# Performance work log

Hardware: AMD Instinct MI355X
Metric: run time of the kernel (lower is better)

The kernel has to match this reference:

```python
import jax, jax.numpy as jnp
import numpy as np

N, S, D = 4, 2048, 1024
H, HD = 16, 64
DF = 3 * D
EPS = 1e-5

def _layernorm(x, g, b):
    mu = jnp.mean(x, axis=-1, keepdims=True)
    var = jnp.mean((x - mu) ** 2, axis=-1, keepdims=True)
    return (x - mu) * jax.lax.rsqrt(var + EPS) * g + b

def _pos_embed(s, d, dtype):
    pos = jnp.arange(s, dtype=dtype)                      # (S,)
    i = jnp.arange(d, dtype=dtype)                        # (D,)
    ang = pos[:, None] / (10000.0 ** (2.0 * i / d))       # (S,D)
    pe = jnp.where((jnp.arange(d) % 2) == 0, jnp.sin(ang), jnp.cos(ang))
    return pe

def setup_inputs() -> dict:
    key = jax.random.key(0)
    ks = jax.random.split(key, 12)
    def w(k, shape, fan_in):
        return jax.random.normal(k, shape, dtype=jnp.float32) * (fan_in ** -0.5)
    return {
        "x":  jax.random.normal(ks[0], (N, S, D), dtype=jnp.float32),
        "Wq": w(ks[1], (D, H * HD), D),
        "Wk": w(ks[2], (D, H * HD), D),
        "Wv": w(ks[3], (D, H * HD), D),
        "Wo": w(ks[4], (H * HD, D), H * HD),
        "W1": w(ks[5], (D, DF), D),
        "b1": jnp.zeros((DF,), dtype=jnp.float32),
        "W2": w(ks[6], (DF, D), DF),
        "b2": jnp.zeros((D,), dtype=jnp.float32),
        "g1": jnp.ones((D,), dtype=jnp.float32),
        "be1": jnp.zeros((D,), dtype=jnp.float32),
        "g2": jnp.ones((D,), dtype=jnp.float32),
        "be2": jnp.zeros((D,), dtype=jnp.float32),
    }

def reference(x, Wq, Wk, Wv, Wo, W1, b1, W2, b2, g1, be1, g2, be2):
    n, s, d = x.shape
    # positional encoding (added to x; note original scales scores by model_dim**0.5)
    x = x + _pos_embed(s, d, x.dtype)[None, :, :]
    # MHA on norm1(x)
    h = _layernorm(x, g1, be1)
    q = (h @ Wq).reshape(n, s, H, HD)
    k = (h @ Wk).reshape(n, s, H, HD)
    v = (h @ Wv).reshape(n, s, H, HD)
    scores = jnp.einsum('bqhd,bkhd->bhqk', q, k) / jnp.sqrt(jnp.asarray(d, x.dtype))
    attn = jax.nn.softmax(scores, axis=-1)
    o = jnp.einsum('bhqk,bkhd->bqhd', attn, v).reshape(n, s, H * HD)
    x = x + o @ Wo
    # FFN on norm2(x): Linear -> LeakyReLU(0.01) -> Linear (dropout = identity in eval)
    h2 = _layernorm(x, g2, be2)
    f = jax.nn.leaky_relu(h2 @ W1 + b1, negative_slope=0.01)
    x = x + (f @ W2 + b2)
    return x
```

## Files before the change

kernel.cpp:

```cpp
#include <hip/hip_runtime.h>

typedef unsigned short u16;
typedef __bf16 bf16x8 __attribute__((ext_vector_type(8)));
typedef float f32x4 __attribute__((ext_vector_type(4)));

__device__ __forceinline__ u16 f2bf(float f) {
  unsigned u = __builtin_bit_cast(unsigned, f);
  u += 0x7FFFu + ((u >> 16) & 1u);
  return (u16)(u >> 16);
}

#define GLOAD16(g, l) __builtin_amdgcn_global_load_lds( \
    (const __attribute__((address_space(1))) unsigned int*)(const void*)(g), \
    (__attribute__((address_space(3))) unsigned int*)(void*)(l), 16, 0, 0)

#define SW(r, c) (((r) << 6) + ((((c) ^ ((r) & 7))) << 3))

__global__ __launch_bounds__(256) void tconv(const float* __restrict__ W,
                                             u16* __restrict__ Wt, int K, int N) {
  __shared__ float t[32][33];
  int n0 = blockIdx.x * 32, k0 = blockIdx.y * 32;
  int tx = threadIdx.x, ty = threadIdx.y;
#pragma unroll
  for (int j = 0; j < 4; ++j)
    t[ty + j * 8][tx] = W[(size_t)(k0 + ty + j * 8) * N + n0 + tx];
  __syncthreads();
#pragma unroll
  for (int j = 0; j < 4; ++j)
    Wt[(size_t)(n0 + ty + j * 8) * K + k0 + tx] = f2bf(t[tx][ty + j * 8]);
}

template <bool PE>
__global__ __launch_bounds__(256) void ln_row(const float* __restrict__ in,
                                              const float* __restrict__ g,
                                              const float* __restrict__ be,
                                              float* __restrict__ xout,
                                              u16* __restrict__ hout) {
  const int row = blockIdx.x;
  const int tid = threadIdx.x;
  const int s = row & 2047;
  float4 xv = *(const float4*)&in[(size_t)row * 1024 + tid * 4];
  float vals[4];
  const float* xp = (const float*)&xv;
#pragma unroll
  for (int j = 0; j < 4; ++j) {
    float v = xp[j];
    if (PE) {
      int d = tid * 4 + j;
      float freq = powf(10000.f, -2.f * (float)d * (1.f / 1024.f));
      float ang = (float)s * freq;
      v += (d & 1) ? cosf(ang) : sinf(ang);
    }
    vals[j] = v;
  }
  if (PE) {
    float4 st;
    float* sp = (float*)&st;
#pragma unroll
    for (int j = 0; j < 4; ++j) sp[j] = vals[j];
    *(float4*)&xout[(size_t)row * 1024 + tid * 4] = st;
  }
  float sum = vals[0] + vals[1] + vals[2] + vals[3];
  float sq = vals[0] * vals[0] + vals[1] * vals[1] + vals[2] * vals[2] + vals[3] * vals[3];
#pragma unroll
  for (int d = 1; d < 64; d <<= 1) {
    sum += __shfl_xor(sum, d);
    sq += __shfl_xor(sq, d);
  }
  __shared__ float red[8];
  int wave = tid >> 6, lane = tid & 63;
  if (lane == 0) { red[wave] = sum; red[4 + wave] = sq; }
  __syncthreads();
  sum = red[0] + red[1] + red[2] + red[3];
  sq = red[4] + red[5] + red[6] + red[7];
  float mu = sum * (1.f / 1024.f);
  float var = sq * (1.f / 1024.f) - mu * mu;
  float rv = rsqrtf(var + 1e-5f);
#pragma unroll
  for (int j = 0; j < 4; ++j) {
    int d = tid * 4 + j;
    hout[(size_t)row * 1024 + d] = f2bf((vals[j] - mu) * rv * g[d] + be[d]);
  }
}

#define EPI_QKV 0
#define EPI_OPROJ 1
#define EPI_FFN1 2
#define EPI_FFN2 3

template <int EPI>
__global__ __launch_bounds__(256, 2) void gemm_bt(
    const u16* __restrict__ A, const u16* __restrict__ Bt, int M, int N, int K,
    const float* __restrict__ bias, const float* __restrict__ resid,
    float* __restrict__ outf, u16* __restrict__ outb,
    u16* __restrict__ oq, u16* __restrict__ okk, u16* __restrict__ ovt) {
  __shared__ __align__(16) u16 As[128 * 32];
  __shared__ __align__(16) u16 Bs[128 * 32];
  const int tid = threadIdx.x;
  const int wave = tid >> 6, lane = tid & 63;
  const int m0 = blockIdx.y * 128, n0 = blockIdx.x * 128;
  const int lrow = lane & 15, kb8 = (lane >> 4) * 8;
  const int wr = (wave >> 1) * 64, wc = (wave & 1) * 64;
  const int srow = tid >> 2, scol = (tid & 3) * 8;
  const u16* Ag = A + (size_t)(m0 + srow) * K + scol;
  const u16* Bg = Bt + (size_t)(n0 + srow) * K + scol;
  u16* asb0 = &As[wave * 512];
  u16* asb1 = &As[2048 + wave * 512];
  u16* bsb0 = &Bs[wave * 512];
  u16* bsb1 = &Bs[2048 + wave * 512];

  f32x4 acc[4][4] = {};

  for (int kt = 0; kt < K; kt += 32) {
    GLOAD16(Ag + kt, asb0);
    GLOAD16(Ag + (size_t)64 * K + kt, asb1);
    GLOAD16(Bg + kt, bsb0);
    GLOAD16(Bg + (size_t)64 * K + kt, bsb1);
    __syncthreads();
    bf16x8 af[4], bfr[4];
#pragma unroll
    for (int m = 0; m < 4; ++m)
      af[m] = *(const bf16x8*)&As[(wr + m * 16 + lrow) * 32 + kb8];
#pragma unroll
    for (int n = 0; n < 4; ++n)
      bfr[n] = *(const bf16x8*)&Bs[(wc + n * 16 + lrow) * 32 + kb8];
#pragma unroll
    for (int m = 0; m < 4; ++m)
#pragma unroll
      for (int n = 0; n < 4; ++n)
        acc[m][n] = __builtin_amdgcn_mfma_f32_16x16x32_bf16(af[m], bfr[n], acc[m][n], 0, 0, 0);
    __syncthreads();
  }

#pragma unroll
  for (int m = 0; m < 4; ++m) {
#pragma unroll
    for (int n = 0; n < 4; ++n) {
#pragma unroll
      for (int i = 0; i < 4; ++i) {
        int row = m0 + wr + m * 16 + (lane >> 4) * 4 + i;
        int col = n0 + wc + n * 16 + lrow;
        float v = acc[m][n][i];
        if (EPI == EPI_QKV) {
          int which = col >> 10, c = col & 1023;
          int h = c >> 6, hd = c & 63;
          int b = row >> 11, s = row & 2047;
          size_t qk = (((size_t)(b * 16 + h) * 2048 + s) << 6) + hd;
          if (which == 0) oq[qk] = f2bf(v * 0.03125f);
          else if (which == 1) okk[qk] = f2bf(v);
          else ovt[((size_t)(b * 16 + h) * 64 + hd) * 2048 + s] = f2bf(v);
        } else if (EPI == EPI_OPROJ) {
          size_t idx = (size_t)row * 1024 + col;
          outf[idx] = v + resid[idx];
        } else if (EPI == EPI_FFN1) {
          float t = v + bias[col];
          t = t > 0.f ? t : 0.01f * t;
          outb[(size_t)row * 3072 + col] = f2bf(t);
        } else {
          size_t idx = (size_t)row * 1024 + col;
          outf[idx] = v + bias[col] + resid[idx];
        }
      }
    }
  }
}

__global__ __launch_bounds__(256, 3) void attn_fwd(const u16* __restrict__ qb,
                                                   const u16* __restrict__ kbuf,
                                                   const u16* __restrict__ vtb,
                                                   u16* __restrict__ ob) {
  __shared__ __align__(16) u16 Kl[2][64 * 64];
  __shared__ __align__(16) u16 Vl[2][64 * 64];
  __shared__ __align__(16) u16 Pl[128 * 64];
  const int tid = threadIdx.x, wave = tid >> 6, lane = tid & 63;
  const int wid = (blockIdx.x & 7) * 128 + (blockIdx.x >> 3);
  const int bh = wid >> 4, qt = wid & 15;
  const int lrow = lane & 15, lhi = lane >> 4;
  const u16* Qg = qb + (((size_t)bh * 2048 + qt * 128) << 6);
  const u16* Kg = kbuf + ((size_t)bh * 2048 << 6);
  const u16* Vg = vtb + (size_t)bh * 64 * 2048;
  const int srow = tid >> 3;
  const int swsrc = ((tid & 7) ^ (srow & 7)) * 8;

#pragma unroll
  for (int j = 0; j < 4; ++j)
    GLOAD16(Qg + (size_t)(srow + j * 32) * 64 + swsrc, &Pl[j * 2048 + wave * 512]);
#pragma unroll
  for (int j = 0; j < 2; ++j) {
    int r = srow + j * 32;
    GLOAD16(Kg + (size_t)r * 64 + swsrc, &Kl[0][j * 2048 + wave * 512]);
    GLOAD16(Vg + (size_t)r * 2048 + swsrc, &Vl[0][j * 2048 + wave * 512]);
  }
  __syncthreads();

  bf16x8 qf[2][2];
#pragma unroll
  for (int m = 0; m < 2; ++m)
#pragma unroll
    for (int kk = 0; kk < 2; ++kk)
      qf[m][kk] = *(const bf16x8*)&Pl[SW(wave * 32 + m * 16 + lrow, kk * 4 + lhi)];

  f32x4 oacc[2][4] = {};
  float lsum[8];
#pragma unroll
  for (int i = 0; i < 8; ++i) lsum[i] = 0.f;

  int cur = 0;
  for (int kv = 0; kv < 2048; kv += 64) {
    if (kv) __syncthreads();
    if (kv + 64 < 2048) {
#pragma unroll
      for (int j = 0; j < 2; ++j) {
        int r = srow + j * 32;
        GLOAD16(Kg + (size_t)(kv + 64 + r) * 64 + swsrc, &Kl[cur ^ 1][j * 2048 + wave * 512]);
        GLOAD16(Vg + (size_t)r * 2048 + kv + 64 + swsrc, &Vl[cur ^ 1][j * 2048 + wave * 512]);
      }
    }

    f32x4 sf[2][4] = {};
#pragma unroll
    for (int n = 0; n < 4; ++n) {
#pragma unroll
      for (int kk = 0; kk < 2; ++kk) {
        bf16x8 kf = *(const bf16x8*)&Kl[cur][SW(n * 16 + lrow, kk * 4 + lhi)];
        sf[0][n] = __builtin_amdgcn_mfma_f32_16x16x32_bf16(qf[0][kk], kf, sf[0][n], 0, 0, 0);
        sf[1][n] = __builtin_amdgcn_mfma_f32_16x16x32_bf16(qf[1][kk], kf, sf[1][n], 0, 0, 0);
      }
    }
#pragma unroll
    for (int m = 0; m < 2; ++m) {
#pragma unroll
      for (int i = 0; i < 4; ++i) {
        float rs = 0.f;
#pragma unroll
        for (int n = 0; n < 4; ++n) {
          float p = __expf(sf[m][n][i]);
          sf[m][n][i] = p;
          rs += p;
        }
        lsum[m * 4 + i] += rs;
      }
    }
#pragma unroll
    for (int m = 0; m < 2; ++m)
#pragma unroll
      for (int n = 0; n < 4; ++n)
#pragma unroll
        for (int i = 0; i < 4; ++i) {
          int pr = wave * 32 + m * 16 + lhi * 4 + i;
          Pl[SW(pr, n * 2 + (lrow >> 3)) + (lrow & 7)] = f2bf(sf[m][n][i]);
        }
#pragma unroll
    for (int kk = 0; kk < 2; ++kk) {
      bf16x8 pf0 = *(const bf16x8*)&Pl[SW(wave * 32 + 0 + lrow, kk * 4 + lhi)];
      bf16x8 pf1 = *(const bf16x8*)&Pl[SW(wave * 32 + 16 + lrow, kk * 4 + lhi)];
#pragma unroll
      for (int n = 0; n < 4; ++n) {
        bf16x8 vf = *(const bf16x8*)&Vl[cur][SW(n * 16 + lrow, kk * 4 + lhi)];
        oacc[0][n] = __builtin_amdgcn_mfma_f32_16x16x32_bf16(pf0, vf, oacc[0][n], 0, 0, 0);
        oacc[1][n] = __builtin_amdgcn_mfma_f32_16x16x32_bf16(pf1, vf, oacc[1][n], 0, 0, 0);
      }
    }
    cur ^= 1;
  }

#pragma unroll
  for (int idx = 0; idx < 8; ++idx)
#pragma unroll
    for (int d = 1; d < 16; d <<= 1)
      lsum[idx] += __shfl_xor(lsum[idx], d, 16);

  const int b = bh >> 4, h = bh & 15;
#pragma unroll
  for (int m = 0; m < 2; ++m)
#pragma unroll
    for (int i = 0; i < 4; ++i) {
      int qrow = qt * 128 + wave * 32 + m * 16 + lhi * 4 + i;
      float inv = 1.f / lsum[m * 4 + i];
#pragma unroll
      for (int n = 0; n < 4; ++n) {
        int hd = n * 16 + lrow;
        ob[((size_t)(b * 2048 + qrow)) * 1024 + h * 64 + hd] = f2bf(oacc[m][n][i] * inv);
      }
    }
}

extern "C" void kernel_launch(void* const* d_in, const int* in_sizes, int n_in,
                              void* d_out, int out_size, void* d_ws, size_t ws_size,
                              hipStream_t stream) {
  const float* x = (const float*)d_in[0];
  const float* Wq = (const float*)d_in[1];
  const float* Wk = (const float*)d_in[2];
  const float* Wv = (const float*)d_in[3];
  const float* Wo = (const float*)d_in[4];
  const float* W1 = (const float*)d_in[5];
  const float* b1 = (const float*)d_in[6];
  const float* W2 = (const float*)d_in[7];
  const float* b2 = (const float*)d_in[8];
  const float* g1 = (const float*)d_in[9];
  const float* be1 = (const float*)d_in[10];
  const float* g2 = (const float*)d_in[11];
  const float* be2 = (const float*)d_in[12];

  char* ws = (char*)d_ws;
  const size_t MB = 1024 * 1024;
  float* x1 = (float*)(ws + 0);
  u16* h = (u16*)(ws + 32 * MB);
  u16* q = (u16*)(ws + 48 * MB);
  u16* k = (u16*)(ws + 64 * MB);
  u16* vt = (u16*)(ws + 80 * MB);
  u16* o = (u16*)(ws + 96 * MB);
  u16* f = (u16*)(ws + 48 * MB);
  u16* wqkv = (u16*)(ws + 112 * MB);
  u16* wo = (u16*)(ws + 118 * MB);
  u16* w1t = (u16*)(ws + 120 * MB);
  u16* w2t = (u16*)(ws + 126 * MB);
  float* out = (float*)d_out;

  dim3 tb(32, 8);
  tconv<<<dim3(32, 32), tb, 0, stream>>>(Wq, wqkv, 1024, 1024);
  tconv<<<dim3(32, 32), tb, 0, stream>>>(Wk, wqkv + 1024 * 1024, 1024, 1024);
  tconv<<<dim3(32, 32), tb, 0, stream>>>(Wv, wqkv + 2 * 1024 * 1024, 1024, 1024);
  tconv<<<dim3(32, 32), tb, 0, stream>>>(Wo, wo, 1024, 1024);
  tconv<<<dim3(96, 32), tb, 0, stream>>>(W1, w1t, 1024, 3072);
  tconv<<<dim3(32, 96), tb, 0, stream>>>(W2, w2t, 3072, 1024);

  ln_row<true><<<8192, 256, 0, stream>>>(x, g1, be1, x1, h);

  gemm_bt<EPI_QKV><<<dim3(24, 64), 256, 0, stream>>>(h, wqkv, 8192, 3072, 1024,
                                                     nullptr, nullptr, nullptr, nullptr,
                                                     q, k, vt);
  attn_fwd<<<1024, 256, 0, stream>>>(q, k, vt, o);

  gemm_bt<EPI_OPROJ><<<dim3(8, 64), 256, 0, stream>>>(o, wo, 8192, 1024, 1024,
                                                      nullptr, x1, x1, nullptr,
                                                      nullptr, nullptr, nullptr);
  ln_row<false><<<8192, 256, 0, stream>>>(x1, g2, be2, nullptr, h);

  gemm_bt<EPI_FFN1><<<dim3(24, 64), 256, 0, stream>>>(h, w1t, 8192, 3072, 1024,
                                                      b1, nullptr, nullptr, f,
                                                      nullptr, nullptr, nullptr);
  gemm_bt<EPI_FFN2><<<dim3(8, 64), 256, 0, stream>>>(f, w2t, 8192, 1024, 3072,
                                                     b2, x1, out, nullptr,
                                                     nullptr, nullptr, nullptr);
}
```

Baseline: 456.6 us.

## Rewrite GEMMs as triple-buffered 256x128 tiles with XOR-swizzled LDS and XCD remap

Replaces the 128x128 single-buffer GEMM with a 512-thread kernel computing 256x128 tiles. It uses a three-stage LDS ring of global_load_lds prefetches with explicit vmcnt waits, so loads overlap MFMA work and only barriers separate stages. It also XOR-swizzles LDS to avoid bank conflicts, remaps blocks across XCDs for locality, and raises wave priority around the MFMAs. This costs more LDS (about 72KB per block) and relies on hand-tuned waitcnt/barrier ordering, which could hide races if miscounted.

After: 473.8 us. 3.8% more time.

```diff
diff --git a/kernel.cpp b/kernel.cpp
--- a/kernel.cpp
+++ b/kernel.cpp
@@ -15,6 +15,13 @@
     (__attribute__((address_space(3))) unsigned int*)(void*)(l), 16, 0, 0)
 
 #define SW(r, c) (((r) << 6) + ((((c) ^ ((r) & 7))) << 3))
+
+#define BARRIER() do { \
+    __builtin_amdgcn_sched_barrier(0); \
+    __builtin_amdgcn_s_barrier(); \
+    asm volatile("" ::: "memory"); \
+    __builtin_amdgcn_sched_barrier(0); \
+  } while (0)
 
 __global__ __launch_bounds__(256) void tconv(const float* __restrict__ W,
                                              u16* __restrict__ Wt, int K, int N) {
@@ -89,48 +96,70 @@
 #define EPI_FFN2 3
 
 template <int EPI>
-__global__ __launch_bounds__(256, 2) void gemm_bt(
-    const u16* __restrict__ A, const u16* __restrict__ Bt, int M, int N, int K,
+__global__ __launch_bounds__(512, 2) void gemm3r(
+    const u16* __restrict__ A, const u16* __restrict__ Bt, int N, int K, int ntx,
     const float* __restrict__ bias, const float* __restrict__ resid,
     float* __restrict__ outf, u16* __restrict__ outb,
     u16* __restrict__ oq, u16* __restrict__ okk, u16* __restrict__ ovt) {
-  __shared__ __align__(16) u16 As[128 * 32];
-  __shared__ __align__(16) u16 Bs[128 * 32];
+  __shared__ __align__(16) u16 Asl[3 * 256 * 32];
+  __shared__ __align__(16) u16 Bsl[3 * 128 * 32];
   const int tid = threadIdx.x;
   const int wave = tid >> 6, lane = tid & 63;
-  const int m0 = blockIdx.y * 128, n0 = blockIdx.x * 128;
-  const int lrow = lane & 15, kb8 = (lane >> 4) * 8;
-  const int wr = (wave >> 1) * 64, wc = (wave & 1) * 64;
-  const int srow = tid >> 2, scol = (tid & 3) * 8;
-  const u16* Ag = A + (size_t)(m0 + srow) * K + scol;
-  const u16* Bg = Bt + (size_t)(n0 + srow) * K + scol;
-  u16* asb0 = &As[wave * 512];
-  u16* asb1 = &As[2048 + wave * 512];
-  u16* bsb0 = &Bs[wave * 512];
-  u16* bsb1 = &Bs[2048 + wave * 512];
+  const int wm = wave >> 1, wn = wave & 1;
+  const int lrow = lane & 15, lhi = lane >> 4;
+  const int nwg = gridDim.x;
+  const int wid = ((int)blockIdx.x & 7) * (nwg >> 3) + ((int)blockIdx.x >> 3);
+  const int m0 = (wid / ntx) * 256, n0 = (wid % ntx) * 128;
+  const int srow = tid >> 2;
+  const int swsrc = (((tid & 3) ^ (srow & 3)) << 3);
+  const int NT = K >> 5;
+
+  const u16* Ag = A + (size_t)(m0 + srow) * K + swsrc;
+  const u16* Bg = Bt + (size_t)(n0 + srow) * K + swsrc;
+  const int rsw = (lrow & 3);
+
+#define STAGE3(bs, kof) do { \
+    GLOAD16(Ag + (kof), &Asl[(bs) * 8192 + (wave * 16) * 32]); \
+    GLOAD16(Ag + (size_t)128 * K + (kof), &Asl[(bs) * 8192 + (128 + wave * 16) * 32]); \
+    GLOAD16(Bg + (kof), &Bsl[(bs) * 4096 + (wave * 16) * 32]); \
+  } while (0)
 
   f32x4 acc[4][4] = {};
 
-  for (int kt = 0; kt < K; kt += 32) {
-    GLOAD16(Ag + kt, asb0);
-    GLOAD16(Ag + (size_t)64 * K + kt, asb1);
-    GLOAD16(Bg + kt, bsb0);
-    GLOAD16(Bg + (size_t)64 * K + kt, bsb1);
-    __syncthreads();
-    bf16x8 af[4], bfr[4];
+  STAGE3(0, 0);
+  STAGE3(1, 32);
+  asm volatile("s_waitcnt vmcnt(3)" ::: "memory");
+  BARRIER();
+
+  int bcur = 0, bst = 2;
+  for (int kt = 0; kt < NT; ++kt) {
+    const int kof2 = (kt + 2 < NT) ? ((kt + 2) << 5) : 0;
+    STAGE3(bst, kof2);
+    const u16* Ab = &Asl[bcur * 8192];
+    const u16* Bb = &Bsl[bcur * 4096];
+    bf16x8 af[4], bfv[4];
 #pragma unroll
     for (int m = 0; m < 4; ++m)
-      af[m] = *(const bf16x8*)&As[(wr + m * 16 + lrow) * 32 + kb8];
+      af[m] = *(const bf16x8*)&Ab[(wm * 64 + m * 16 + lrow) * 32 + ((lhi ^ rsw) << 3)];
 #pragma unroll
     for (int n = 0; n < 4; ++n)
-      bfr[n] = *(const bf16x8*)&Bs[(wc + n * 16 + lrow) * 32 + kb8];
+      bfv[n] = *(const bf16x8*)&Bb[(wn * 64 + n * 16 + lrow) * 32 + ((lhi ^ rsw) << 3)];
+    asm volatile("s_waitcnt vmcnt(3)" ::: "memory");
+    BARRIER();
+    asm volatile("s_waitcnt lgkmcnt(0)" ::: "memory");
+    __builtin_amdgcn_sched_barrier(0);
+    __builtin_amdgcn_s_setprio(1);
 #pragma unroll
     for (int m = 0; m < 4; ++m)
 #pragma unroll
       for (int n = 0; n < 4; ++n)
-        acc[m][n] = __builtin_amdgcn_mfma_f32_16x16x32_bf16(af[m], bfr[n], acc[m][n], 0, 0, 0);
-    __syncthreads();
-  }
+        acc[m][n] = __builtin_amdgcn_mfma_f32_16x16x32_bf16(af[m], bfv[n], acc[m][n], 0, 0, 0);
+    __builtin_amdgcn_s_setprio(0);
+    BARRIER();
+    bcur = (bcur == 2) ? 0 : bcur + 1;
+    bst = (bst == 2) ? 0 : bst + 1;
+  }
+  asm volatile("s_waitcnt vmcnt(0)" ::: "memory");
 
 #pragma unroll
   for (int m = 0; m < 4; ++m) {
@@ -138,8 +167,8 @@
     for (int n = 0; n < 4; ++n) {
 #pragma unroll
       for (int i = 0; i < 4; ++i) {
-        int row = m0 + wr + m * 16 + (lane >> 4) * 4 + i;
-        int col = n0 + wc + n * 16 + lrow;
+        int row = m0 + wm * 64 + m * 16 + lhi * 4 + i;
+        int col = n0 + wn * 64 + n * 16 + lrow;
         float v = acc[m][n][i];
         if (EPI == EPI_QKV) {
           int which = col >> 10, c = col & 1023;
@@ -163,6 +192,7 @@
       }
     }
   }
+#undef STAGE3
 }
 
 __global__ __launch_bounds__(256, 3) void attn_fwd(const u16* __restrict__ qb,
@@ -327,20 +357,20 @@
 
   ln_row<true><<<8192, 256, 0, stream>>>(x, g1, be1, x1, h);
 
-  gemm_bt<EPI_QKV><<<dim3(24, 64), 256, 0, stream>>>(h, wqkv, 8192, 3072, 1024,
-                                                     nullptr, nullptr, nullptr, nullptr,
-                                                     q, k, vt);
+  gemm3r<EPI_QKV><<<768, 512, 0, stream>>>(h, wqkv, 3072, 1024, 24,
+                                           nullptr, nullptr, nullptr, nullptr,
+                                           q, k, vt);
   attn_fwd<<<1024, 256, 0, stream>>>(q, k, vt, o);
 
-  gemm_bt<EPI_OPROJ><<<dim3(8, 64), 256, 0, stream>>>(o, wo, 8192, 1024, 1024,
-                                                      nullptr, x1, x1, nullptr,
-                                                      nullptr, nullptr, nullptr);
+  gemm3r<EPI_OPROJ><<<256, 512, 0, stream>>>(o, wo, 1024, 1024, 8,
+                                             nullptr, x1, x1, nullptr,
+                                             nullptr, nullptr, nullptr);
   ln_row<false><<<8192, 256, 0, stream>>>(x1, g2, be2, nullptr, h);
 
-  gemm_bt<EPI_FFN1><<<dim3(24, 64), 256, 0, stream>>>(h, w1t, 8192, 3072, 1024,
-                                                      b1, nullptr, nullptr, f,
-                                                      nullptr, nullptr, nullptr);
-  gemm_bt<EPI_FFN2><<<dim3(8, 64), 256, 0, stream>>>(f, w2t, 8192, 1024, 3072,
-                                                     b2, x1, out, nullptr,
-                                                     nullptr, nullptr, nullptr);
-}
+  gemm3r<EPI_FFN1><<<768, 512, 0, stream>>>(h, w1t, 3072, 1024, 24,
+                                            b1, nullptr, nullptr, f,
+                                            nullptr, nullptr, nullptr);
+  gemm3r<EPI_FFN2><<<256, 512, 0, stream>>>(f, w2t, 1024, 3072, 8,
+                                            b2, x1, out, nullptr,
+                                            nullptr, nullptr, nullptr);
+}
```

## Replace GEMM with 256x256-tile, 8-wave, multi-buffered pipelined bf16 kernel

Applied to the files above, without the earlier changes.

Replaces the 128x128 single-buffered GEMM with a 512-thread kernel that computes 256x256 output tiles. It uses double-buffered, split-K LDS staging with swizzled layout, explicit vmcnt waits and barriers so global-to-LDS loads overlap the MFMA phases, and s_setprio around the math. It also remaps workgroup IDs in chunks of 8, presumably for XCD locality. The aim is higher operand reuse and latency hiding across all four GEMMs, at the cost of more registers and LDS and one block per CU. OPROJ and FFN2 launch only 128 blocks, which may underfill the GPU.

Result: slower. 492.5 us (+7.9%).

```diff
diff --git a/kernel.cpp b/kernel.cpp
--- a/kernel.cpp
+++ b/kernel.cpp
@@ -89,58 +89,104 @@
 #define EPI_FFN2 3
 
 template <int EPI>
-__global__ __launch_bounds__(256, 2) void gemm_bt(
-    const u16* __restrict__ A, const u16* __restrict__ Bt, int M, int N, int K,
+__global__ __launch_bounds__(512, 1) void gemm8p(
+    const u16* __restrict__ A, const u16* __restrict__ Bt, int K, int ntx,
     const float* __restrict__ bias, const float* __restrict__ resid,
     float* __restrict__ outf, u16* __restrict__ outb,
     u16* __restrict__ oq, u16* __restrict__ okk, u16* __restrict__ ovt) {
-  __shared__ __align__(16) u16 As[128 * 32];
-  __shared__ __align__(16) u16 Bs[128 * 32];
+  __shared__ __align__(16) u16 Als[2][2][8192];
+  __shared__ __align__(16) u16 Bls[2][2][8192];
   const int tid = threadIdx.x;
   const int wave = tid >> 6, lane = tid & 63;
-  const int m0 = blockIdx.y * 128, n0 = blockIdx.x * 128;
-  const int lrow = lane & 15, kb8 = (lane >> 4) * 8;
-  const int wr = (wave >> 1) * 64, wc = (wave & 1) * 64;
-  const int srow = tid >> 2, scol = (tid & 3) * 8;
-  const u16* Ag = A + (size_t)(m0 + srow) * K + scol;
-  const u16* Bg = Bt + (size_t)(n0 + srow) * K + scol;
-  u16* asb0 = &As[wave * 512];
-  u16* asb1 = &As[2048 + wave * 512];
-  u16* bsb0 = &Bs[wave * 512];
-  u16* bsb1 = &Bs[2048 + wave * 512];
-
-  f32x4 acc[4][4] = {};
-
-  for (int kt = 0; kt < K; kt += 32) {
-    GLOAD16(Ag + kt, asb0);
-    GLOAD16(Ag + (size_t)64 * K + kt, asb1);
-    GLOAD16(Bg + kt, bsb0);
-    GLOAD16(Bg + (size_t)64 * K + kt, bsb1);
-    __syncthreads();
-    bf16x8 af[4], bfr[4];
-#pragma unroll
-    for (int m = 0; m < 4; ++m)
-      af[m] = *(const bf16x8*)&As[(wr + m * 16 + lrow) * 32 + kb8];
-#pragma unroll
-    for (int n = 0; n < 4; ++n)
-      bfr[n] = *(const bf16x8*)&Bs[(wc + n * 16 + lrow) * 32 + kb8];
-#pragma unroll
-    for (int m = 0; m < 4; ++m)
-#pragma unroll
-      for (int n = 0; n < 4; ++n)
-        acc[m][n] = __builtin_amdgcn_mfma_f32_16x16x32_bf16(af[m], bfr[n], acc[m][n], 0, 0, 0);
-    __syncthreads();
-  }
-
-#pragma unroll
-  for (int m = 0; m < 4; ++m) {
-#pragma unroll
-    for (int n = 0; n < 4; ++n) {
+  const int wm = wave >> 2, wn = wave & 3;
+  const int lrow = lane & 15, lhi = lane >> 4;
+  const int nwg = gridDim.x;
+  const int wid = ((int)blockIdx.x & 7) * (nwg >> 3) + ((int)blockIdx.x >> 3);
+  const int m0 = (wid / ntx) * 256, n0 = (wid % ntx) * 256;
+  const int NT = K >> 6, NIT = NT >> 1;
+
+  const int u = (lane & 7) ^ ((lane >> 3) & 7);
+  const int srow2 = wave * 8 + (lane >> 3);
+  const size_t aR0 = (size_t)(m0 + 2 * srow2 + (u >> 2)) * K + (u & 3) * 8;
+  const size_t aR1 = aR0 + (size_t)128 * K;
+  const size_t bR0 = (size_t)(n0 + 2 * srow2 + (u >> 2)) * K + (u & 3) * 8;
+  const size_t bR1 = bR0 + (size_t)128 * K;
+  const int jchk = ((lrow >> 1) << 6) + (((((lrow & 1) << 2) + lhi) ^ ((lrow >> 1) & 7)) << 3);
+
+#define STG_A(b, kk, kof) do { \
+    GLOAD16(A + aR0 + (kof) + (kk) * 32, &Als[b][kk][wave * 512]); \
+    GLOAD16(A + aR1 + (kof) + (kk) * 32, &Als[b][kk][4096 + wave * 512]); \
+  } while (0)
+#define STG_B(b, kk, kof) do { \
+    GLOAD16(Bt + bR0 + (kof) + (kk) * 32, &Bls[b][kk][wave * 512]); \
+    GLOAD16(Bt + bR1 + (kof) + (kk) * 32, &Bls[b][kk][4096 + wave * 512]); \
+  } while (0)
+#define VM4 asm volatile("s_waitcnt vmcnt(4)" ::: "memory")
+
+  f32x4 acc[8][4] = {};
+  bf16x8 afr[4], bfr[4];
+
+#define PHASE(TB, KK, MH, READB, STGSTMT, ENDVM) do { \
+    if (READB) { \
+      _Pragma("unroll") \
+      for (int nf = 0; nf < 4; ++nf) \
+        bfr[nf] = *(const bf16x8*)&Bls[TB][KK][wn * 2048 + nf * 512 + jchk]; \
+    } \
+    _Pragma("unroll") \
+    for (int a = 0; a < 4; ++a) \
+      afr[a] = *(const bf16x8*)&Als[TB][KK][wm * 4096 + ((MH) * 4 + a) * 512 + jchk]; \
+    STGSTMT; \
+    __builtin_amdgcn_sched_barrier(0); \
+    __builtin_amdgcn_s_barrier(); \
+    asm volatile("s_waitcnt lgkmcnt(0)" ::: "memory"); \
+    __builtin_amdgcn_sched_barrier(0); \
+    __builtin_amdgcn_s_setprio(1); \
+    _Pragma("unroll") \
+    for (int a = 0; a < 4; ++a) \
+      _Pragma("unroll") \
+      for (int nf = 0; nf < 4; ++nf) \
+        acc[(MH) * 4 + a][nf] = \
+            __builtin_amdgcn_mfma_f32_16x16x32_bf16(afr[a], bfr[nf], acc[(MH) * 4 + a][nf], 0, 0, 0); \
+    __builtin_amdgcn_s_setprio(0); \
+    __builtin_amdgcn_sched_barrier(0); \
+    ENDVM; \
+    __builtin_amdgcn_s_barrier(); \
+    asm volatile("" ::: "memory"); \
+    __builtin_amdgcn_sched_barrier(0); \
+  } while (0)
+
+  STG_A(0, 0, 0); STG_B(0, 0, 0);
+  STG_A(0, 1, 0); STG_B(0, 1, 0);
+  STG_A(1, 0, 64); STG_B(1, 0, 64);
+  VM4;
+  __builtin_amdgcn_s_barrier();
+  asm volatile("" ::: "memory");
+
+  for (int it = 0; it < NIT; ++it) {
+    const int kof1 = (2 * it + 1) << 6;
+    const int t2 = 2 * it + 2, t3 = 2 * it + 3;
+    const int kof2 = (t2 < NT) ? (t2 << 6) : 0;
+    const int kof3 = (t3 < NT) ? (t3 << 6) : 0;
+    PHASE(0, 0, 0, 1, STG_A(1, 1, kof1), );
+    PHASE(0, 0, 1, 0, STG_B(1, 1, kof1), );
+    PHASE(0, 1, 0, 1, STG_A(0, 0, kof2), );
+    PHASE(0, 1, 1, 0, STG_B(0, 0, kof2), VM4);
+    PHASE(1, 0, 0, 1, STG_A(0, 1, kof2), );
+    PHASE(1, 0, 1, 0, STG_B(0, 1, kof2), );
+    PHASE(1, 1, 0, 1, STG_A(1, 0, kof3), );
+    PHASE(1, 1, 1, 0, STG_B(1, 0, kof3), VM4);
+  }
+  asm volatile("s_waitcnt vmcnt(0)" ::: "memory");
+
+#pragma unroll
+  for (int mf = 0; mf < 8; ++mf) {
+#pragma unroll
+    for (int nf = 0; nf < 4; ++nf) {
 #pragma unroll
       for (int i = 0; i < 4; ++i) {
-        int row = m0 + wr + m * 16 + (lane >> 4) * 4 + i;
-        int col = n0 + wc + n * 16 + lrow;
-        float v = acc[m][n][i];
+        int row = m0 + wm * 128 + mf * 16 + lhi * 4 + i;
+        int col = n0 + wn * 64 + nf * 16 + lrow;
+        float v = acc[mf][nf][i];
         if (EPI == EPI_QKV) {
           int which = col >> 10, c = col & 1023;
           int h = c >> 6, hd = c & 63;
@@ -163,6 +209,10 @@
       }
     }
   }
+#undef PHASE
+#undef STG_A
+#undef STG_B
+#undef VM4
 }
 
 __global__ __launch_bounds__(256, 3) void attn_fwd(const u16* __restrict__ qb,
@@ -327,20 +377,20 @@
 
   ln_row<true><<<8192, 256, 0, stream>>>(x, g1, be1, x1, h);
 
-  gemm_bt<EPI_QKV><<<dim3(24, 64), 256, 0, stream>>>(h, wqkv, 8192, 3072, 1024,
-                                                     nullptr, nullptr, nullptr, nullptr,
-                                                     q, k, vt);
+  gemm8p<EPI_QKV><<<384, 512, 0, stream>>>(h, wqkv, 1024, 12,
+                                           nullptr, nullptr, nullptr, nullptr,
+                                           q, k, vt);
   attn_fwd<<<1024, 256, 0, stream>>>(q, k, vt, o);
 
-  gemm_bt<EPI_OPROJ><<<dim3(8, 64), 256, 0, stream>>>(o, wo, 8192, 1024, 1024,
-                                                      nullptr, x1, x1, nullptr,
-                                                      nullptr, nullptr, nullptr);
+  gemm8p<EPI_OPROJ><<<128, 512, 0, stream>>>(o, wo, 1024, 4,
+                                             nullptr, x1, x1, nullptr,
+                                             nullptr, nullptr, nullptr);
   ln_row<false><<<8192, 256, 0, stream>>>(x1, g2, be2, nullptr, h);
 
-  gemm_bt<EPI_FFN1><<<dim3(24, 64), 256, 0, stream>>>(h, w1t, 8192, 3072, 1024,
-                                                      b1, nullptr, nullptr, f,
-                                                      nullptr, nullptr, nullptr);
-  gemm_bt<EPI_FFN2><<<dim3(8, 64), 256, 0, stream>>>(f, w2t, 8192, 1024, 3072,
-                                                     b2, x1, out, nullptr,
-                                                     nullptr, nullptr, nullptr);
-}
+  gemm8p<EPI_FFN1><<<384, 512, 0, stream>>>(h, w1t, 1024, 12,
+                                            b1, nullptr, nullptr, f,
+                                            nullptr, nullptr, nullptr);
+  gemm8p<EPI_FFN2><<<128, 512, 0, stream>>>(f, w2t, 3072, 4,
+                                            b2, x1, out, nullptr,
+                                            nullptr, nullptr, nullptr);
+}
```

## Double GEMM k-tile to 64 with XOR-swizzled LDS layout

Applied to the files above, without the earlier changes.

The bf16 GEMM now stages 64-wide K slices per iteration instead of 32. That halves the number of loop iterations and barrier pairs and issues eight direct global-to-LDS loads per thread. The LDS rows are XOR-swizzled, applied on the global source column and on the fragment read address, to avoid bank conflicts on the wider rows. LDS use doubles to 32 KB per block, which may cap occupancy at the declared two blocks per CU. Each iteration also holds twice as many fragment registers.

After: 433.8 us. 5.0% less time.

```diff
diff --git a/kernel.cpp b/kernel.cpp
--- a/kernel.cpp
+++ b/kernel.cpp
@@ -94,41 +94,44 @@
     const float* __restrict__ bias, const float* __restrict__ resid,
     float* __restrict__ outf, u16* __restrict__ outb,
     u16* __restrict__ oq, u16* __restrict__ okk, u16* __restrict__ ovt) {
-  __shared__ __align__(16) u16 As[128 * 32];
-  __shared__ __align__(16) u16 Bs[128 * 32];
+  __shared__ __align__(16) u16 As[128 * 64];
+  __shared__ __align__(16) u16 Bs[128 * 64];
   const int tid = threadIdx.x;
   const int wave = tid >> 6, lane = tid & 63;
   const int m0 = blockIdx.y * 128, n0 = blockIdx.x * 128;
-  const int lrow = lane & 15, kb8 = (lane >> 4) * 8;
+  const int lrow = lane & 15, lhi = lane >> 4;
   const int wr = (wave >> 1) * 64, wc = (wave & 1) * 64;
-  const int srow = tid >> 2, scol = (tid & 3) * 8;
-  const u16* Ag = A + (size_t)(m0 + srow) * K + scol;
-  const u16* Bg = Bt + (size_t)(n0 + srow) * K + scol;
-  u16* asb0 = &As[wave * 512];
-  u16* asb1 = &As[2048 + wave * 512];
-  u16* bsb0 = &Bs[wave * 512];
-  u16* bsb1 = &Bs[2048 + wave * 512];
+  const int srow = tid >> 3;
+  const int swsrc = ((tid & 7) ^ (srow & 7)) * 8;
+  const u16* Ag = A + (size_t)(m0 + srow) * K + swsrc;
+  const u16* Bg = Bt + (size_t)(n0 + srow) * K + swsrc;
 
   f32x4 acc[4][4] = {};
 
-  for (int kt = 0; kt < K; kt += 32) {
-    GLOAD16(Ag + kt, asb0);
-    GLOAD16(Ag + (size_t)64 * K + kt, asb1);
-    GLOAD16(Bg + kt, bsb0);
-    GLOAD16(Bg + (size_t)64 * K + kt, bsb1);
+  for (int kt = 0; kt < K; kt += 64) {
+#pragma unroll
+    for (int j = 0; j < 4; ++j) {
+      GLOAD16(Ag + (size_t)(j * 32) * K + kt, &As[j * 2048 + wave * 512]);
+      GLOAD16(Bg + (size_t)(j * 32) * K + kt, &Bs[j * 2048 + wave * 512]);
+    }
     __syncthreads();
-    bf16x8 af[4], bfr[4];
-#pragma unroll
-    for (int m = 0; m < 4; ++m)
-      af[m] = *(const bf16x8*)&As[(wr + m * 16 + lrow) * 32 + kb8];
-#pragma unroll
-    for (int n = 0; n < 4; ++n)
-      bfr[n] = *(const bf16x8*)&Bs[(wc + n * 16 + lrow) * 32 + kb8];
-#pragma unroll
-    for (int m = 0; m < 4; ++m)
+    bf16x8 af[2][4], bfr[2][4];
+#pragma unroll
+    for (int kk = 0; kk < 2; ++kk) {
+#pragma unroll
+      for (int m = 0; m < 4; ++m)
+        af[kk][m] = *(const bf16x8*)&As[SW(wr + m * 16 + lrow, kk * 4 + lhi)];
 #pragma unroll
       for (int n = 0; n < 4; ++n)
-        acc[m][n] = __builtin_amdgcn_mfma_f32_16x16x32_bf16(af[m], bfr[n], acc[m][n], 0, 0, 0);
+        bfr[kk][n] = *(const bf16x8*)&Bs[SW(wc + n * 16 + lrow, kk * 4 + lhi)];
+    }
+#pragma unroll
+    for (int kk = 0; kk < 2; ++kk)
+#pragma unroll
+      for (int m = 0; m < 4; ++m)
+#pragma unroll
+        for (int n = 0; n < 4; ++n)
+          acc[m][n] = __builtin_amdgcn_mfma_f32_16x16x32_bf16(af[kk][m], bfr[kk][n], acc[m][n], 0, 0, 0);
     __syncthreads();
   }
 
@@ -138,7 +141,7 @@
     for (int n = 0; n < 4; ++n) {
 #pragma unroll
       for (int i = 0; i < 4; ++i) {
-        int row = m0 + wr + m * 16 + (lane >> 4) * 4 + i;
+        int row = m0 + wr + m * 16 + lhi * 4 + i;
         int col = n0 + wc + n * 16 + lrow;
         float v = acc[m][n][i];
         if (EPI == EPI_QKV) {
```
